# Performance work log

Measured on AMD Instinct MI355X. Metric: run time of the kernel, lower is better.

## Reference

```python
import jax, jax.numpy as jnp
import numpy as np

B, D, H, W, C = 2, 8, 56, 56, 384
NH = 12
HD = C // NH
WIN = (2, 7, 7)
SHIFT = (1, 3, 3)
TDIM = 384
RANK = C // 8
HID = 4 * C
N = WIN[0] * WIN[1] * WIN[2]  # 98 tokens per window
NW = (D // WIN[0]) * (H // WIN[1]) * (W // WIN[2])  # windows per batch element


def _rel_index():
    wd, wh, ww = WIN
    coords = np.stack(np.meshgrid(np.arange(wd), np.arange(wh), np.arange(ww), indexing='ij'))
    coords = coords.reshape(3, -1)  # (3, N)
    rel = (coords[:, :, None] - coords[:, None, :]).transpose(1, 2, 0)  # (N, N, 3)
    rel[..., 0] += wd - 1; rel[..., 1] += wh - 1; rel[..., 2] += ww - 1
    rel[..., 0] *= (2 * wh - 1) * (2 * ww - 1)
    rel[..., 1] *= (2 * ww - 1)
    return rel.sum(-1)  # (N, N) int

REL_IDX = _rel_index()


def _wpart_np(x):
    b, d, h, w, c = x.shape
    x = x.reshape(b, d // WIN[0], WIN[0], h // WIN[1], WIN[1], w // WIN[2], WIN[2], c)
    return x.transpose(0, 1, 3, 5, 2, 4, 6, 7).reshape(-1, N, c)


def _attn_mask():
    # faithful port of compute_mask (note: only 2 slices along W, as in source)
    wd, wh, ww = WIN
    sd, sh, sw = SHIFT
    img = np.zeros((1, D, H, W, 1), np.float32)
    cnt = 0
    for ds in (slice(-wd), slice(-wd, -sd), slice(-sd, None)):
        for hs in (slice(-wh), slice(-wh, -sh), slice(-sh, None)):
            for ws in (slice(-ww), slice(-ww, None)):
                img[:, ds, hs, ws, :] = cnt
                cnt += 1
    mw = _wpart_np(img).squeeze(-1)  # (nW, N)
    am = mw[:, None, :] - mw[:, :, None]  # (nW, N, N)
    return np.where(am != 0, np.float32(-100.0), np.float32(0.0))

ATTN_MASK = _attn_mask()


def wpart(x):
    b, c = x.shape[0], x.shape[-1]
    x = x.reshape(b, D // WIN[0], WIN[0], H // WIN[1], WIN[1], W // WIN[2], WIN[2], c)
    return x.transpose(0, 1, 3, 5, 2, 4, 6, 7).reshape(-1, N, c)


def wrev(win):
    c = win.shape[-1]
    x = win.reshape(B, D // WIN[0], H // WIN[1], W // WIN[2], WIN[0], WIN[1], WIN[2], c)
    return x.transpose(0, 1, 4, 2, 5, 3, 6, 7).reshape(B, D, H, W, c)


def ln(x):
    m = x.mean(-1, keepdims=True)
    v = ((x - m) ** 2).mean(-1, keepdims=True)
    return (x - m) / jnp.sqrt(v + 1e-6)


def window_attn(xw, qkv_w, qkv_b, proj_w, proj_b, rel_bias, mask):
    Bw = xw.shape[0]
    qkv = (xw @ qkv_w + qkv_b).reshape(Bw, N, 3, NH, HD).transpose(2, 0, 3, 1, 4)
    q, k, v = qkv[0] * (HD ** -0.5), qkv[1], qkv[2]
    a = jnp.einsum('bhnd,bhmd->bhnm', q, k)  # (Bw, NH, N, N)
    bias = rel_bias[REL_IDX.reshape(-1)].reshape(N, N, NH).transpose(2, 0, 1)
    a = a + bias[None]
    a = a.reshape(Bw // NW, NW, NH, N, N) + mask[None, :, None]
    a = jax.nn.softmax(a.reshape(Bw, NH, N, N), axis=-1)
    out = jnp.einsum('bhnm,bhmd->bhnd', a, v).transpose(0, 2, 1, 3).reshape(Bw, N, C)
    return out @ proj_w + proj_b


def setup_inputs() -> dict:
    key = jax.random.key(0)
    ks = jax.random.split(key, 16)
    s = 0.02
    return {
        'x': jax.random.normal(ks[0], (B, D, H, W, C), jnp.float32),
        't': jax.random.normal(ks[1], (B, TDIM), jnp.float32),
        'qkv_w': jax.random.normal(ks[2], (C, 3 * C), jnp.float32) * s,
        'qkv_b': jax.random.normal(ks[3], (3 * C,), jnp.float32) * s,
        'proj_w': jax.random.normal(ks[4], (C, C), jnp.float32) * s,
        'proj_b': jax.random.normal(ks[5], (C,), jnp.float32) * s,
        'rel_bias': jax.random.normal(ks[6], ((2 * WIN[0] - 1) * (2 * WIN[1] - 1) * (2 * WIN[2] - 1), NH), jnp.float32) * s,
        'fc1_w': jax.random.normal(ks[7], (C, HID), jnp.float32) * s,
        'fc1_b': jax.random.normal(ks[8], (HID,), jnp.float32) * s,
        'fc2_w': jax.random.normal(ks[9], (HID, C), jnp.float32) * s,
        'fc2_b': jax.random.normal(ks[10], (C,), jnp.float32) * s,
        'ada_w1': jax.random.normal(ks[11], (TDIM, RANK), jnp.float32) * s,
        'ada_w2': jax.random.normal(ks[12], (RANK, 6 * C), jnp.float32) * s,
        'ada_b2': jax.random.normal(ks[13], (6 * C,), jnp.float32) * s,
    }


def reference(x, t, qkv_w, qkv_b, proj_w, proj_b, rel_bias, fc1_w, fc1_b, fc2_w, fc2_b, ada_w1, ada_w2, ada_b2):
    mask = jnp.asarray(ATTN_MASK)
    mod = jax.nn.silu(t) @ ada_w1 @ ada_w2 + ada_b2  # (B, 6C)
    s_msa, sc_msa, g_msa, s_mlp, sc_mlp, g_mlp = jnp.split(mod, 6, axis=1)

    def mod5(h, sh, sc):
        return h * (1 + sc[:, None, None, None, :]) + sh[:, None, None, None, :]

    # attention branch (shifted-window MSA)
    h = mod5(ln(x), s_msa, sc_msa)
    hs = jnp.roll(h, shift=(-SHIFT[0], -SHIFT[1], -SHIFT[2]), axis=(1, 2, 3))
    aw = window_attn(wpart(hs), qkv_w, qkv_b, proj_w, proj_b, rel_bias, mask)
    hs = wrev(aw)
    h = jnp.roll(hs, shift=SHIFT, axis=(1, 2, 3))
    x = x + g_msa[:, None, None, None, :] * h

    # MLP branch
    h2 = mod5(ln(x), s_mlp, sc_mlp)
    m = jax.nn.gelu(h2 @ fc1_w + fc1_b, approximate=False) @ fc2_w + fc2_b
    return x + g_mlp[:, None, None, None, :] * m
```

## Files before the change

### kernel.cpp

```cpp
#include <hip/hip_runtime.h>
#include <hip/hip_bf16.h>
#include <math.h>

using bf16 = __hip_bfloat16;
typedef __bf16 bf16x8 __attribute__((ext_vector_type(8)));
typedef float f32x4 __attribute__((ext_vector_type(4)));
typedef unsigned int u32;


__device__ __forceinline__ void async_cp16(const void* g, void* l) {
  __builtin_amdgcn_global_load_lds(
      (const __attribute__((address_space(1))) u32*)g,
      (__attribute__((address_space(3))) u32*)l, 16, 0, 0);
}

__device__ __forceinline__ int row_to_gidx(int row) {
  int win = row / 98, tok = row - win * 98;
  int b = win >> 8, wd = (win >> 6) & 3, wh = (win >> 3) & 7, ww = win & 7;
  int td = tok / 49, rem = tok - td * 49;
  int th = rem / 7, tw = rem - th * 7;
  int od = (wd * 2 + td + 1) & 7;
  int oh = wh * 7 + th + 3; if (oh >= 56) oh -= 56;
  int ow = ww * 7 + tw + 3; if (ow >= 56) ow -= 56;
  return ((b * 8 + od) * 56 + oh) * 56 + ow;
}

__global__ __launch_bounds__(256) void mod_kernel(
    const float* __restrict__ t, const float* __restrict__ w1,
    const float* __restrict__ w2, const float* __restrict__ b2,
    float* __restrict__ modout)
{
  __shared__ float u[2 * 48];
  int tid = threadIdx.x;
  if (tid < 96) {
    int b = tid / 48, r = tid - (tid / 48) * 48;
    float acc = 0.f;
    for (int k = 0; k < 384; ++k) {
      float x = t[b * 384 + k];
      float s = x / (1.f + __expf(-x));
      acc += s * w1[k * 48 + r];
    }
    u[b * 48 + r] = acc;
  }
  __syncthreads();
  for (int idx = tid; idx < 2 * 2304; idx += 256) {
    int b = idx / 2304, c = idx - b * 2304;
    float acc = b2[c];
    #pragma unroll
    for (int k = 0; k < 48; ++k) acc += u[b * 48 + k] * w2[k * 2304 + c];
    modout[idx] = acc;
  }
}

__global__ __launch_bounds__(256) void wconv_kernel(
    const float* __restrict__ W, bf16* __restrict__ Wt, int K, int N)
{
  int idx = blockIdx.x * 256 + threadIdx.x;
  if (idx < K * N) {
    int k = idx / N, n = idx - k * N;
    Wt[(size_t)n * K + k] = __float2bfloat16(W[idx]);
  }
}

__global__ __launch_bounds__(256) void bm_kernel(
    const float* __restrict__ relb, bf16* __restrict__ bm)
{
  int idx = blockIdx.x * 256 + threadIdx.x;
  if (idx >= 4 * 12 * 112 * 112) return;
  int j = idx % 112, tmp = idx / 112;
  int i = tmp % 112; tmp /= 112;
  int h = tmp % 12, p = tmp / 12;
  float v;
  if (i < 98 && j < 98) {
    int tdi = i / 49, ri = i % 49, thi = ri / 7, twi = ri % 7;
    int tdj = j / 49, rj = j % 49, thj = rj / 7, twj = rj % 7;
    int ridx = (tdi - tdj + 1) * 169 + (thi - thj + 6) * 13 + (twi - twj + 6);
    bool msk = ((p & 2) && (tdi != tdj)) || ((p & 1) && ((thi < 4) != (thj < 4)));
    v = relb[ridx * 12 + h] + (msk ? -100.f : 0.f);
  } else {
    v = -1e38f;
  }
  bm[idx] = __float2bfloat16(v);
}

template <int PHASE>
__global__ __launch_bounds__(256) void ln_mod_kernel(
    const float* __restrict__ src, const float* __restrict__ modv,
    bf16* __restrict__ dst)
{
  int wid = threadIdx.x >> 6, lane = threadIdx.x & 63;
  int row = blockIdx.x * 4 + wid;
  int gtok;
  if (PHASE == 0) gtok = row_to_gidx(row); else gtok = row;
  int b = row / 25088;
  const float* s = src + (size_t)gtok * 384;
  float vals[6], sum = 0.f, sq = 0.f;
  #pragma unroll
  for (int i = 0; i < 6; ++i) {
    float v = s[lane + i * 64];
    vals[i] = v; sum += v; sq += v * v;
  }
  #pragma unroll
  for (int o = 32; o; o >>= 1) { sum += __shfl_xor(sum, o, 64); sq += __shfl_xor(sq, o, 64); }
  float mean = sum * (1.f / 384.f);
  float var = sq * (1.f / 384.f) - mean * mean;
  float rstd = rsqrtf(var + 1e-6f);
  int mb = b * 2304 + (PHASE == 0 ? 0 : 1152);
  #pragma unroll
  for (int i = 0; i < 6; ++i) {
    int c = lane + i * 64;
    float scv = modv[mb + 384 + c], shv = modv[mb + c];
    dst[(size_t)row * 384 + c] = __float2bfloat16((vals[i] - mean) * rstd * (1.f + scv) + shv);
  }
}

template <int EPI>
__global__ __launch_bounds__(256) void gemm128_kernel(
    const bf16* __restrict__ A, const bf16* __restrict__ Bt,
    const float* __restrict__ bias, const int N, const int K,
    bf16* __restrict__ outB, float* __restrict__ outF,
    const float* __restrict__ resid, const float* __restrict__ modv)
{
  __shared__ bf16 sA[2][128 * 32];
  __shared__ bf16 sB[2][128 * 32];
  const int tid = threadIdx.x;
  const int lane = tid & 63, wid = tid >> 6;
  const int wm = wid >> 1, wn = wid & 1;

  const int gx = gridDim.x;
  const int nwg = gx * (int)gridDim.y;
  const int orig = (int)blockIdx.y * gx + (int)blockIdx.x;
  const int q = nwg >> 3;
  const int wg = (orig & 7) * q + (orig >> 3);
  const int bx = wg % gx, by = wg / gx;
  const int row0 = by * 128, col0 = bx * 128;

  const int lrow = lane & 15;
  const int sl8 = (((lane >> 4) ^ ((lane >> 1) & 3)) << 3);
  const int r0 = tid >> 2;
  const int c0 = (((tid & 3) ^ ((tid >> 3) & 3)) << 3);

  const f32x4 vzero = {0.f, 0.f, 0.f, 0.f};
  f32x4 acc[4][4];
  #pragma unroll
  for (int m = 0; m < 4; ++m)
    #pragma unroll
    for (int n = 0; n < 4; ++n) acc[m][n] = vzero;

  const bf16* Arow0 = A + (size_t)(row0 + r0) * K + c0;
  const bf16* Arow1 = A + (size_t)(row0 + r0 + 64) * K + c0;
  const bf16* Brow0 = Bt + (size_t)(col0 + r0) * K + c0;
  const bf16* Brow1 = Bt + (size_t)(col0 + r0 + 64) * K + c0;

  auto stage = [&](int b, int kt) {
    async_cp16(Arow0 + kt, &sA[b][(size_t)tid * 8]);
    async_cp16(Arow1 + kt, &sA[b][(size_t)(tid + 256) * 8]);
    async_cp16(Brow0 + kt, &sB[b][(size_t)tid * 8]);
    async_cp16(Brow1 + kt, &sB[b][(size_t)(tid + 256) * 8]);
  };
  auto compute = [&](int cb) {
    bf16x8 af[4], bfv[4];
    #pragma unroll
    for (int m = 0; m < 4; ++m)
      af[m] = *(const bf16x8*)(&sA[cb][(wm * 64 + m * 16 + lrow) * 32 + sl8]);
    #pragma unroll
    for (int n = 0; n < 4; ++n)
      bfv[n] = *(const bf16x8*)(&sB[cb][(wn * 64 + n * 16 + lrow) * 32 + sl8]);
    #pragma unroll
    for (int m = 0; m < 4; ++m)
      #pragma unroll
      for (int n = 0; n < 4; ++n)
        acc[m][n] = __builtin_amdgcn_mfma_f32_16x16x32_bf16(af[m], bfv[n], acc[m][n], 0, 0, 0);
  };

  stage(0, 0);
  asm volatile("s_waitcnt vmcnt(0)" ::: "memory");
  __syncthreads();
  int cur = 0;
  for (int kt = 32; kt < K; kt += 32) {
    stage(cur ^ 1, kt);
    compute(cur);
    asm volatile("s_waitcnt vmcnt(0)" ::: "memory");
    __syncthreads();
    cur ^= 1;
  }
  compute(cur);

  #pragma unroll
  for (int m = 0; m < 4; ++m) {
    #pragma unroll
    for (int r = 0; r < 4; ++r) {
      const int row = row0 + wm * 64 + m * 16 + (lane >> 4) * 4 + r;
      int gofs = 0, b = 0;
      if (EPI == 1) { gofs = row_to_gidx(row) * 384; b = row / 25088; }
      if (EPI == 3) { gofs = row * 384; b = row / 25088; }
      #pragma unroll
      for (int n = 0; n < 4; ++n) {
        const int col = col0 + wn * 64 + n * 16 + (lane & 15);
        float v = acc[m][n][r] + bias[col];
        if (EPI == 0) {
          outB[(size_t)row * N + col] = __float2bfloat16(v);
        } else if (EPI == 2) {
          float g = 0.5f * v * (1.f + erff(v * 0.70710678118654752f));
          outB[(size_t)row * N + col] = __float2bfloat16(g);
        } else if (EPI == 1) {
          outF[gofs + col] = resid[gofs + col] + modv[b * 2304 + 768 + col] * v;
        } else {
          outF[gofs + col] = resid[gofs + col] + modv[b * 2304 + 1920 + col] * v;
        }
      }
    }
  }
}

__global__ __launch_bounds__(256) void attn_kernel(
    const bf16* __restrict__ qkv, const bf16* __restrict__ bm,
    bf16* __restrict__ outp)
{
  __shared__ bf16 k_s[112][40];
  __shared__ bf16 v_t[32][136];
  __shared__ bf16 p_s[4][16][136];

  const int head = blockIdx.x;
  const int win = blockIdx.y;
  const int tid = threadIdx.x;
  const int lane = tid & 63, wid = tid >> 6;
  const int g = lane >> 4, c16 = lane & 15;
  const size_t rowbase = (size_t)win * 98;
  const bf16 zero = __float2bfloat16(0.f);

  for (int lin = tid; lin < 448; lin += 256) {
    int row = lin >> 2, ch = (lin & 3) << 3;
    uint4 val = make_uint4(0, 0, 0, 0);
    if (row < 98)
      val = *(const uint4*)(qkv + (rowbase + row) * 1152 + 384 + head * 32 + ch);
    *(uint4*)&k_s[row][ch] = val;
  }
  for (int lin = tid; lin < 4096; lin += 256) {
    int d = lin & 31, tok = lin >> 5;
    bf16 val = zero;
    if (tok < 98) val = qkv[(rowbase + tok) * 1152 + 768 + head * 32 + d];
    v_t[d][tok] = val;
  }
  for (int lin = tid; lin < 1536; lin += 256) {
    int w = lin / 384, rem = lin - w * 384;
    p_s[w][rem / 24][112 + rem % 24] = zero;
  }
  __syncthreads();

  const int p = ((((win >> 6) & 3) == 3) ? 2 : 0) | ((((win >> 3) & 7) == 7) ? 1 : 0);
  const bf16* bmrow = bm + (size_t)(p * 12 + head) * 12544;
  const float scale = 0.17677669529663687f;
  const f32x4 vzero = {0.f, 0.f, 0.f, 0.f};

  for (int s = wid; s < 7; s += 4) {
    const int q0 = s * 16;
    int qrow = q0 + c16; if (qrow > 97) qrow = 97;
    bf16x8 qf = *(const bf16x8*)(qkv + (rowbase + qrow) * 1152 + head * 32 + g * 8);

    f32x4 sa[7];
    #pragma unroll
    for (int ct = 0; ct < 7; ++ct) {
      bf16x8 kf = *(const bf16x8*)&k_s[ct * 16 + c16][g * 8];
      sa[ct] = __builtin_amdgcn_mfma_f32_16x16x32_bf16(qf, kf, vzero, 0, 0, 0);
    }

    float sv[7][4];
    float mrow[4] = {-1e30f, -1e30f, -1e30f, -1e30f};
    #pragma unroll
    for (int ct = 0; ct < 7; ++ct) {
      #pragma unroll
      for (int r = 0; r < 4; ++r) {
        int i = q0 + g * 4 + r, j = ct * 16 + c16;
        float val = sa[ct][r] * scale + __bfloat162float(bmrow[i * 112 + j]);
        sv[ct][r] = val;
        mrow[r] = fmaxf(mrow[r], val);
      }
    }
    #pragma unroll
    for (int r = 0; r < 4; ++r) {
      #pragma unroll
      for (int off = 1; off < 16; off <<= 1)
        mrow[r] = fmaxf(mrow[r], __shfl_xor(mrow[r], off, 64));
    }
    float rsum[4] = {0.f, 0.f, 0.f, 0.f};
    #pragma unroll
    for (int ct = 0; ct < 7; ++ct) {
      #pragma unroll
      for (int r = 0; r < 4; ++r) {
        float e = __expf(sv[ct][r] - mrow[r]);
        sv[ct][r] = e;
        rsum[r] += e;
      }
    }
    #pragma unroll
    for (int r = 0; r < 4; ++r) {
      #pragma unroll
      for (int off = 1; off < 16; off <<= 1)
        rsum[r] += __shfl_xor(rsum[r], off, 64);
      rsum[r] = 1.f / rsum[r];
    }
    #pragma unroll
    for (int ct = 0; ct < 7; ++ct)
      #pragma unroll
      for (int r = 0; r < 4; ++r)
        p_s[wid][g * 4 + r][ct * 16 + c16] = __float2bfloat16(sv[ct][r] * rsum[r]);

    asm volatile("s_waitcnt lgkmcnt(0)" ::: "memory");

    f32x4 o0 = vzero, o1 = vzero;
    #pragma unroll
    for (int kk = 0; kk < 4; ++kk) {
      bf16x8 pa = *(const bf16x8*)&p_s[wid][c16][kk * 32 + g * 8];
      bf16x8 v0 = *(const bf16x8*)&v_t[c16][kk * 32 + g * 8];
      bf16x8 v1 = *(const bf16x8*)&v_t[16 + c16][kk * 32 + g * 8];
      o0 = __builtin_amdgcn_mfma_f32_16x16x32_bf16(pa, v0, o0, 0, 0, 0);
      o1 = __builtin_amdgcn_mfma_f32_16x16x32_bf16(pa, v1, o1, 0, 0, 0);
    }
    #pragma unroll
    for (int r = 0; r < 4; ++r) {
      int qi = q0 + g * 4 + r;
      if (qi < 98) {
        size_t ob = (rowbase + qi) * 384 + head * 32;
        outp[ob + c16] = __float2bfloat16(o0[r]);
        outp[ob + 16 + c16] = __float2bfloat16(o1[r]);
      }
    }
  }
}

extern "C" void kernel_launch(void* const* d_in, const int* in_sizes, int n_in,
                              void* d_out, int out_size, void* d_ws, size_t ws_size,
                              hipStream_t stream)
{
  (void)in_sizes; (void)n_in; (void)out_size; (void)ws_size;
  const float* x      = (const float*)d_in[0];
  const float* t      = (const float*)d_in[1];
  const float* qkv_w  = (const float*)d_in[2];
  const float* qkv_b  = (const float*)d_in[3];
  const float* proj_w = (const float*)d_in[4];
  const float* proj_b = (const float*)d_in[5];
  const float* relb   = (const float*)d_in[6];
  const float* fc1_w  = (const float*)d_in[7];
  const float* fc1_b  = (const float*)d_in[8];
  const float* fc2_w  = (const float*)d_in[9];
  const float* fc2_b  = (const float*)d_in[10];
  const float* ada_w1 = (const float*)d_in[11];
  const float* ada_w2 = (const float*)d_in[12];
  const float* ada_b2 = (const float*)d_in[13];
  float* out = (float*)d_out;
  char* ws = (char*)d_ws;

  float* modbuf = (float*)(ws + 0);
  bf16* wqkv_t  = (bf16*)(ws + 18432);
  bf16* wproj_t = (bf16*)(ws + 903168);
  bf16* wfc1_t  = (bf16*)(ws + 1198080);
  bf16* wfc2_t  = (bf16*)(ws + 2377728);
  bf16* bufA    = (bf16*)(ws + 3557376);
  bf16* qkvbuf  = (bf16*)(ws + 42092544);
  bf16* bufB    = (bf16*)(ws + 42092544 + 115605504);
  bf16* midbuf  = (bf16*)(ws + 42092544);
  bf16* bmbuf   = bufA;

  wconv_kernel<<<(384 * 1152 + 255) / 256, 256, 0, stream>>>(qkv_w, wqkv_t, 384, 1152);
  wconv_kernel<<<(384 * 384 + 255) / 256, 256, 0, stream>>>(proj_w, wproj_t, 384, 384);
  wconv_kernel<<<(384 * 1536 + 255) / 256, 256, 0, stream>>>(fc1_w, wfc1_t, 384, 1536);
  wconv_kernel<<<(1536 * 384 + 255) / 256, 256, 0, stream>>>(fc2_w, wfc2_t, 1536, 384);

  mod_kernel<<<1, 256, 0, stream>>>(t, ada_w1, ada_w2, ada_b2, modbuf);

  ln_mod_kernel<0><<<12544, 256, 0, stream>>>(x, modbuf, bufA);

  gemm128_kernel<0><<<dim3(9, 392), 256, 0, stream>>>(bufA, wqkv_t, qkv_b, 1152, 384,
                                                      qkvbuf, nullptr, nullptr, nullptr);

  bm_kernel<<<2352, 256, 0, stream>>>(relb, bmbuf);

  attn_kernel<<<dim3(12, 512), 256, 0, stream>>>(qkvbuf, bmbuf, bufB);

  gemm128_kernel<1><<<dim3(3, 392), 256, 0, stream>>>(bufB, wproj_t, proj_b, 384, 384,
                                                      nullptr, out, x, modbuf);

  ln_mod_kernel<1><<<12544, 256, 0, stream>>>(out, modbuf, bufA);

  gemm128_kernel<2><<<dim3(12, 392), 256, 0, stream>>>(bufA, wfc1_t, fc1_b, 1536, 384,
                                                       midbuf, nullptr, nullptr, nullptr);

  gemm128_kernel<3><<<dim3(3, 392), 256, 0, stream>>>(midbuf, wfc2_t, fc2_b, 384, 1536,
                                                      nullptr, out, out, modbuf);
}
```

Before: 566.2 us.

## Triple-buffer GEMM K-loop, transpose MFMA operands for vectorized epilogue stores

```diff
diff --git a/kernel.cpp b/kernel.cpp
--- a/kernel.cpp
+++ b/kernel.cpp
@@ -4,6 +4,7 @@
 
 using bf16 = __hip_bfloat16;
 typedef __bf16 bf16x8 __attribute__((ext_vector_type(8)));
+typedef __bf16 bf16x4 __attribute__((ext_vector_type(4)));
 typedef float f32x4 __attribute__((ext_vector_type(4)));
 typedef unsigned int u32;
 
@@ -115,14 +116,14 @@
 }
 
 template <int EPI>
-__global__ __launch_bounds__(256) void gemm128_kernel(
+__global__ __launch_bounds__(256, 3) void gemm128_kernel(
     const bf16* __restrict__ A, const bf16* __restrict__ Bt,
     const float* __restrict__ bias, const int N, const int K,
     bf16* __restrict__ outB, float* __restrict__ outF,
     const float* __restrict__ resid, const float* __restrict__ modv)
 {
-  __shared__ bf16 sA[2][128 * 32];
-  __shared__ bf16 sB[2][128 * 32];
+  __shared__ bf16 sA[3][128 * 32];
+  __shared__ bf16 sB[3][128 * 32];
   const int tid = threadIdx.x;
   const int lane = tid & 63, wid = tid >> 6;
   const int wm = wid >> 1, wn = wid & 1;
@@ -130,8 +131,9 @@
   const int gx = gridDim.x;
   const int nwg = gx * (int)gridDim.y;
   const int orig = (int)blockIdx.y * gx + (int)blockIdx.x;
-  const int q = nwg >> 3;
-  const int wg = (orig & 7) * q + (orig >> 3);
+  const int q = nwg >> 3, rr = nwg & 7;
+  const int xcd = orig & 7, idx = orig >> 3;
+  const int wg = (xcd < rr ? xcd * (q + 1) : rr * (q + 1) + (xcd - rr) * q) + idx;
   const int bx = wg % gx, by = wg / gx;
   const int row0 = by * 128, col0 = bx * 128;
 
@@ -170,44 +172,61 @@
     for (int m = 0; m < 4; ++m)
       #pragma unroll
       for (int n = 0; n < 4; ++n)
-        acc[m][n] = __builtin_amdgcn_mfma_f32_16x16x32_bf16(af[m], bfv[n], acc[m][n], 0, 0, 0);
+        acc[m][n] = __builtin_amdgcn_mfma_f32_16x16x32_bf16(bfv[n], af[m], acc[m][n], 0, 0, 0);
   };
 
+  const int nk = K >> 5;
   stage(0, 0);
-  asm volatile("s_waitcnt vmcnt(0)" ::: "memory");
-  __syncthreads();
-  int cur = 0;
-  for (int kt = 32; kt < K; kt += 32) {
-    stage(cur ^ 1, kt);
-    compute(cur);
-    asm volatile("s_waitcnt vmcnt(0)" ::: "memory");
-    __syncthreads();
-    cur ^= 1;
-  }
-  compute(cur);
-
+  stage(1, 32);
+  int cb = 0, st = 2;
+  for (int t = 0; t < nk; ++t) {
+    if (t + 1 < nk) asm volatile("s_waitcnt vmcnt(4)" ::: "memory");
+    else            asm volatile("s_waitcnt vmcnt(0)" ::: "memory");
+    __builtin_amdgcn_s_barrier();
+    __builtin_amdgcn_sched_barrier(0);
+    if (t + 2 < nk) {
+      stage(st, (t + 2) * 32);
+      st = (st == 2) ? 0 : st + 1;
+    }
+    compute(cb);
+    cb = (cb == 2) ? 0 : cb + 1;
+  }
+
+  const int cg = (lane >> 4) << 2;
   #pragma unroll
   for (int m = 0; m < 4; ++m) {
-    #pragma unroll
-    for (int r = 0; r < 4; ++r) {
-      const int row = row0 + wm * 64 + m * 16 + (lane >> 4) * 4 + r;
-      int gofs = 0, b = 0;
-      if (EPI == 1) { gofs = row_to_gidx(row) * 384; b = row / 25088; }
-      if (EPI == 3) { gofs = row * 384; b = row / 25088; }
-      #pragma unroll
-      for (int n = 0; n < 4; ++n) {
-        const int col = col0 + wn * 64 + n * 16 + (lane & 15);
-        float v = acc[m][n][r] + bias[col];
-        if (EPI == 0) {
-          outB[(size_t)row * N + col] = __float2bfloat16(v);
-        } else if (EPI == 2) {
-          float g = 0.5f * v * (1.f + erff(v * 0.70710678118654752f));
-          outB[(size_t)row * N + col] = __float2bfloat16(g);
-        } else if (EPI == 1) {
-          outF[gofs + col] = resid[gofs + col] + modv[b * 2304 + 768 + col] * v;
-        } else {
-          outF[gofs + col] = resid[gofs + col] + modv[b * 2304 + 1920 + col] * v;
+    const int row = row0 + wm * 64 + m * 16 + lrow;
+    int gofs = 0, b = 0;
+    if (EPI == 1) { gofs = row_to_gidx(row) * 384; b = row / 25088; }
+    if (EPI == 3) { gofs = row * 384; b = row / 25088; }
+    #pragma unroll
+    for (int n = 0; n < 4; ++n) {
+      const int colb = col0 + wn * 64 + n * 16 + cg;
+      const f32x4 bi = *(const f32x4*)(bias + colb);
+      f32x4 v;
+      #pragma unroll
+      for (int r = 0; r < 4; ++r) v[r] = acc[m][n][r] + bi[r];
+      if (EPI == 0) {
+        bf16x4 pk;
+        #pragma unroll
+        for (int r = 0; r < 4; ++r) pk[r] = (__bf16)v[r];
+        *(bf16x4*)(outB + (size_t)row * N + colb) = pk;
+      } else if (EPI == 2) {
+        bf16x4 pk;
+        #pragma unroll
+        for (int r = 0; r < 4; ++r) {
+          float g = 0.5f * v[r] * (1.f + erff(v[r] * 0.70710678118654752f));
+          pk[r] = (__bf16)g;
         }
+        *(bf16x4*)(outB + (size_t)row * N + colb) = pk;
+      } else {
+        const int mo = b * 2304 + (EPI == 1 ? 768 : 1920);
+        const f32x4 res = *(const f32x4*)(resid + gofs + colb);
+        const f32x4 gm = *(const f32x4*)(modv + mo + colb);
+        f32x4 o;
+        #pragma unroll
+        for (int r = 0; r < 4; ++r) o[r] = res[r] + gm[r] * v[r];
+        *(f32x4*)(outF + gofs + colb) = o;
       }
     }
   }
```

Result: slower. 585.7 us (+3.4%).

## Fuse QKV projection GEMM into windowed attention kernel per window

Applied to the files above, without the earlier changes.

```diff
diff --git a/kernel.cpp b/kernel.cpp
--- a/kernel.cpp
+++ b/kernel.cpp
@@ -213,119 +213,180 @@
   }
 }
 
-__global__ __launch_bounds__(256) void attn_kernel(
-    const bf16* __restrict__ qkv, const bf16* __restrict__ bm,
+__global__ __launch_bounds__(256) void qkv_attn_kernel(
+    const bf16* __restrict__ A, const bf16* __restrict__ Wqkv,
+    const float* __restrict__ qkv_b, const bf16* __restrict__ bm,
     bf16* __restrict__ outp)
 {
+  __shared__ bf16 q_s[112][40];
   __shared__ bf16 k_s[112][40];
   __shared__ bf16 v_t[32][136];
   __shared__ bf16 p_s[4][16][136];
 
-  const int head = blockIdx.x;
-  const int win = blockIdx.y;
+  const int win = blockIdx.x;
   const int tid = threadIdx.x;
   const int lane = tid & 63, wid = tid >> 6;
   const int g = lane >> 4, c16 = lane & 15;
   const size_t rowbase = (size_t)win * 98;
   const bf16 zero = __float2bfloat16(0.f);
-
-  for (int lin = tid; lin < 448; lin += 256) {
-    int row = lin >> 2, ch = (lin & 3) << 3;
-    uint4 val = make_uint4(0, 0, 0, 0);
-    if (row < 98)
-      val = *(const uint4*)(qkv + (rowbase + row) * 1152 + 384 + head * 32 + ch);
-    *(uint4*)&k_s[row][ch] = val;
-  }
-  for (int lin = tid; lin < 4096; lin += 256) {
-    int d = lin & 31, tok = lin >> 5;
-    bf16 val = zero;
-    if (tok < 98) val = qkv[(rowbase + tok) * 1152 + 768 + head * 32 + d];
-    v_t[d][tok] = val;
-  }
+  const f32x4 vzero = {0.f, 0.f, 0.f, 0.f};
+
+  for (int lin = tid; lin < 768; lin += 256)
+    v_t[lin / 24][112 + lin % 24] = zero;
   for (int lin = tid; lin < 1536; lin += 256) {
     int w = lin / 384, rem = lin - w * 384;
     p_s[w][rem / 24][112 + rem % 24] = zero;
   }
+
+  bf16x8 af[2][12];
+  #pragma unroll
+  for (int si = 0; si < 2; ++si) {
+    const int s = wid + si * 4;
+    int srow = s * 16 + c16; if (srow > 97) srow = 97;
+    const bf16* ap = A + (rowbase + srow) * 384 + g * 8;
+    #pragma unroll
+    for (int ks = 0; ks < 12; ++ks)
+      af[si][ks] = *(const bf16x8*)(ap + ks * 32);
+  }
+
+  const int p = ((((win >> 6) & 3) == 3) ? 2 : 0) | ((((win >> 3) & 7) == 7) ? 1 : 0);
+  const float scale = 0.17677669529663687f;
+
   __syncthreads();
 
-  const int p = ((((win >> 6) & 3) == 3) ? 2 : 0) | ((((win >> 3) & 7) == 7) ? 1 : 0);
-  const bf16* bmrow = bm + (size_t)(p * 12 + head) * 12544;
-  const float scale = 0.17677669529663687f;
-  const f32x4 vzero = {0.f, 0.f, 0.f, 0.f};
-
-  for (int s = wid; s < 7; s += 4) {
-    const int q0 = s * 16;
-    int qrow = q0 + c16; if (qrow > 97) qrow = 97;
-    bf16x8 qf = *(const bf16x8*)(qkv + (rowbase + qrow) * 1152 + head * 32 + g * 8);
-
-    f32x4 sa[7];
-    #pragma unroll
-    for (int ct = 0; ct < 7; ++ct) {
-      bf16x8 kf = *(const bf16x8*)&k_s[ct * 16 + c16][g * 8];
-      sa[ct] = __builtin_amdgcn_mfma_f32_16x16x32_bf16(qf, kf, vzero, 0, 0, 0);
+  for (int h = 0; h < 12; ++h) {
+    f32x4 acc[2][3][2];
+    #pragma unroll
+    for (int si = 0; si < 2; ++si)
+      #pragma unroll
+      for (int mat = 0; mat < 3; ++mat)
+        #pragma unroll
+        for (int nt = 0; nt < 2; ++nt) acc[si][mat][nt] = vzero;
+
+    const bf16* wp = Wqkv + ((size_t)(h * 32 + c16)) * 384 + g * 8;
+    #pragma unroll
+    for (int ks = 0; ks < 12; ++ks) {
+      bf16x8 bfr[3][2];
+      #pragma unroll
+      for (int mat = 0; mat < 3; ++mat)
+        #pragma unroll
+        for (int nt = 0; nt < 2; ++nt)
+          bfr[mat][nt] = *(const bf16x8*)(wp + (size_t)(mat * 384 + nt * 16) * 384 + ks * 32);
+      #pragma unroll
+      for (int si = 0; si < 2; ++si)
+        #pragma unroll
+        for (int mat = 0; mat < 3; ++mat)
+          #pragma unroll
+          for (int nt = 0; nt < 2; ++nt)
+            acc[si][mat][nt] = __builtin_amdgcn_mfma_f32_16x16x32_bf16(
+                af[si][ks], bfr[mat][nt], acc[si][mat][nt], 0, 0, 0);
     }
 
-    float sv[7][4];
-    float mrow[4] = {-1e30f, -1e30f, -1e30f, -1e30f};
-    #pragma unroll
-    for (int ct = 0; ct < 7; ++ct) {
+    #pragma unroll
+    for (int si = 0; si < 2; ++si) {
+      const int s = wid + si * 4;
+      if (s < 7) {
+        #pragma unroll
+        for (int mat = 0; mat < 3; ++mat) {
+          const float b0 = qkv_b[mat * 384 + h * 32 + c16];
+          const float b1 = qkv_b[mat * 384 + h * 32 + 16 + c16];
+          #pragma unroll
+          for (int r = 0; r < 4; ++r) {
+            const int tok = s * 16 + g * 4 + r;
+            const float v0 = acc[si][mat][0][r] + b0;
+            const float v1 = acc[si][mat][1][r] + b1;
+            if (mat == 0) {
+              q_s[tok][c16] = __float2bfloat16(v0);
+              q_s[tok][16 + c16] = __float2bfloat16(v1);
+            } else if (mat == 1) {
+              k_s[tok][c16] = __float2bfloat16(v0);
+              k_s[tok][16 + c16] = __float2bfloat16(v1);
+            } else {
+              const bool ok = tok < 98;
+              v_t[c16][tok] = ok ? __float2bfloat16(v0) : zero;
+              v_t[16 + c16][tok] = ok ? __float2bfloat16(v1) : zero;
+            }
+          }
+        }
+      }
+    }
+    __syncthreads();
+
+    const bf16* bmrow = bm + (size_t)(p * 12 + h) * 12544;
+    for (int s = wid; s < 7; s += 4) {
+      const int q0 = s * 16;
+      bf16x8 qf = *(const bf16x8*)&q_s[q0 + c16][g * 8];
+
+      f32x4 sa[7];
+      #pragma unroll
+      for (int ct = 0; ct < 7; ++ct) {
+        bf16x8 kf = *(const bf16x8*)&k_s[ct * 16 + c16][g * 8];
+        sa[ct] = __builtin_amdgcn_mfma_f32_16x16x32_bf16(qf, kf, vzero, 0, 0, 0);
+      }
+
+      float sv[7][4];
+      float mrow[4] = {-1e30f, -1e30f, -1e30f, -1e30f};
+      #pragma unroll
+      for (int ct = 0; ct < 7; ++ct) {
+        #pragma unroll
+        for (int r = 0; r < 4; ++r) {
+          int i = q0 + g * 4 + r, j = ct * 16 + c16;
+          float val = sa[ct][r] * scale + __bfloat162float(bmrow[i * 112 + j]);
+          sv[ct][r] = val;
+          mrow[r] = fmaxf(mrow[r], val);
+        }
+      }
       #pragma unroll
       for (int r = 0; r < 4; ++r) {
-        int i = q0 + g * 4 + r, j = ct * 16 + c16;
-        float val = sa[ct][r] * scale + __bfloat162float(bmrow[i * 112 + j]);
-        sv[ct][r] = val;
-        mrow[r] = fmaxf(mrow[r], val);
+        #pragma unroll
+        for (int off = 1; off < 16; off <<= 1)
+          mrow[r] = fmaxf(mrow[r], __shfl_xor(mrow[r], off, 64));
+      }
+      float rsum[4] = {0.f, 0.f, 0.f, 0.f};
+      #pragma unroll
+      for (int ct = 0; ct < 7; ++ct) {
+        #pragma unroll
+        for (int r = 0; r < 4; ++r) {
+          float e = __expf(sv[ct][r] - mrow[r]);
+          sv[ct][r] = e;
+          rsum[r] += e;
+        }
+      }
+      #pragma unroll
+      for (int r = 0; r < 4; ++r) {
+        #pragma unroll
+        for (int off = 1; off < 16; off <<= 1)
+          rsum[r] += __shfl_xor(rsum[r], off, 64);
+        rsum[r] = 1.f / rsum[r];
+      }
+      #pragma unroll
+      for (int ct = 0; ct < 7; ++ct)
+        #pragma unroll
+        for (int r = 0; r < 4; ++r)
+          p_s[wid][g * 4 + r][ct * 16 + c16] = __float2bfloat16(sv[ct][r] * rsum[r]);
+
+      asm volatile("s_waitcnt lgkmcnt(0)" ::: "memory");
+
+      f32x4 o0 = vzero, o1 = vzero;
+      #pragma unroll
+      for (int kk = 0; kk < 4; ++kk) {
+        bf16x8 pa = *(const bf16x8*)&p_s[wid][c16][kk * 32 + g * 8];
+        bf16x8 v0 = *(const bf16x8*)&v_t[c16][kk * 32 + g * 8];
+        bf16x8 v1 = *(const bf16x8*)&v_t[16 + c16][kk * 32 + g * 8];
+        o0 = __builtin_amdgcn_mfma_f32_16x16x32_bf16(pa, v0, o0, 0, 0, 0);
+        o1 = __builtin_amdgcn_mfma_f32_16x16x32_bf16(pa, v1, o1, 0, 0, 0);
+      }
+      #pragma unroll
+      for (int r = 0; r < 4; ++r) {
+        int qi = q0 + g * 4 + r;
+        if (qi < 98) {
+          size_t ob = (rowbase + qi) * 384 + h * 32;
+          outp[ob + c16] = __float2bfloat16(o0[r]);
+          outp[ob + 16 + c16] = __float2bfloat16(o1[r]);
+        }
       }
     }
-    #pragma unroll
-    for (int r = 0; r < 4; ++r) {
-      #pragma unroll
-      for (int off = 1; off < 16; off <<= 1)
-        mrow[r] = fmaxf(mrow[r], __shfl_xor(mrow[r], off, 64));
-    }
-    float rsum[4] = {0.f, 0.f, 0.f, 0.f};
-    #pragma unroll
-    for (int ct = 0; ct < 7; ++ct) {
-      #pragma unroll
-      for (int r = 0; r < 4; ++r) {
-        float e = __expf(sv[ct][r] - mrow[r]);
-        sv[ct][r] = e;
-        rsum[r] += e;
-      }
-    }
-    #pragma unroll
-    for (int r = 0; r < 4; ++r) {
-      #pragma unroll
-      for (int off = 1; off < 16; off <<= 1)
-        rsum[r] += __shfl_xor(rsum[r], off, 64);
-      rsum[r] = 1.f / rsum[r];
-    }
-    #pragma unroll
-    for (int ct = 0; ct < 7; ++ct)
-      #pragma unroll
-      for (int r = 0; r < 4; ++r)
-        p_s[wid][g * 4 + r][ct * 16 + c16] = __float2bfloat16(sv[ct][r] * rsum[r]);
-
-    asm volatile("s_waitcnt lgkmcnt(0)" ::: "memory");
-
-    f32x4 o0 = vzero, o1 = vzero;
-    #pragma unroll
-    for (int kk = 0; kk < 4; ++kk) {
-      bf16x8 pa = *(const bf16x8*)&p_s[wid][c16][kk * 32 + g * 8];
-      bf16x8 v0 = *(const bf16x8*)&v_t[c16][kk * 32 + g * 8];
-      bf16x8 v1 = *(const bf16x8*)&v_t[16 + c16][kk * 32 + g * 8];
-      o0 = __builtin_amdgcn_mfma_f32_16x16x32_bf16(pa, v0, o0, 0, 0, 0);
-      o1 = __builtin_amdgcn_mfma_f32_16x16x32_bf16(pa, v1, o1, 0, 0, 0);
-    }
-    #pragma unroll
-    for (int r = 0; r < 4; ++r) {
-      int qi = q0 + g * 4 + r;
-      if (qi < 98) {
-        size_t ob = (rowbase + qi) * 384 + head * 32;
-        outp[ob + c16] = __float2bfloat16(o0[r]);
-        outp[ob + 16 + c16] = __float2bfloat16(o1[r]);
-      }
-    }
+    __syncthreads();
   }
 }
 
@@ -357,10 +418,9 @@
   bf16* wfc1_t  = (bf16*)(ws + 1198080);
   bf16* wfc2_t  = (bf16*)(ws + 2377728);
   bf16* bufA    = (bf16*)(ws + 3557376);
-  bf16* qkvbuf  = (bf16*)(ws + 42092544);
-  bf16* bufB    = (bf16*)(ws + 42092544 + 115605504);
+  bf16* bufB    = (bf16*)(ws + 42092544);
   bf16* midbuf  = (bf16*)(ws + 42092544);
-  bf16* bmbuf   = bufA;
+  bf16* bmbuf   = (bf16*)(ws + 195028992);
 
   wconv_kernel<<<(384 * 1152 + 255) / 256, 256, 0, stream>>>(qkv_w, wqkv_t, 384, 1152);
   wconv_kernel<<<(384 * 384 + 255) / 256, 256, 0, stream>>>(proj_w, wproj_t, 384, 384);
@@ -368,15 +428,11 @@
   wconv_kernel<<<(1536 * 384 + 255) / 256, 256, 0, stream>>>(fc2_w, wfc2_t, 1536, 384);
 
   mod_kernel<<<1, 256, 0, stream>>>(t, ada_w1, ada_w2, ada_b2, modbuf);
+  bm_kernel<<<2352, 256, 0, stream>>>(relb, bmbuf);
 
   ln_mod_kernel<0><<<12544, 256, 0, stream>>>(x, modbuf, bufA);
 
-  gemm128_kernel<0><<<dim3(9, 392), 256, 0, stream>>>(bufA, wqkv_t, qkv_b, 1152, 384,
-                                                      qkvbuf, nullptr, nullptr, nullptr);
-
-  bm_kernel<<<2352, 256, 0, stream>>>(relb, bmbuf);
-
-  attn_kernel<<<dim3(12, 512), 256, 0, stream>>>(qkvbuf, bmbuf, bufB);
+  qkv_attn_kernel<<<512, 256, 0, stream>>>(bufA, wqkv_t, qkv_b, bmbuf, bufB);
 
   gemm128_kernel<1><<<dim3(3, 392), 256, 0, stream>>>(bufB, wproj_t, proj_b, 384, 384,
                                                       nullptr, out, x, modbuf);
```

Result: slower. 735.7 us (+29.9%).

## Pre-pack weights into MFMA fragment layout and load B directly from global

Applied to the files above, without the earlier changes.

```diff
diff --git a/kernel.cpp b/kernel.cpp
--- a/kernel.cpp
+++ b/kernel.cpp
@@ -52,14 +52,16 @@
   }
 }
 
-__global__ __launch_bounds__(256) void wconv_kernel(
-    const float* __restrict__ W, bf16* __restrict__ Wt, int K, int N)
+__global__ __launch_bounds__(256) void wconv_frag_kernel(
+    const float* __restrict__ W, bf16* __restrict__ Wf, int K, int N)
 {
   int idx = blockIdx.x * 256 + threadIdx.x;
-  if (idx < K * N) {
-    int k = idx / N, n = idx - k * N;
-    Wt[(size_t)n * K + k] = __float2bfloat16(W[idx]);
-  }
+  if (idx >= K * N) return;
+  int k = idx / N, n = idx - (idx / N) * N;
+  int ntile = n >> 4, kstep = k >> 5;
+  int l = (n & 15) + (((k >> 3) & 3) << 4);
+  size_t dst = (((size_t)(ntile * (K >> 5) + kstep)) << 9) + (l << 3) + (k & 7);
+  Wf[dst] = __float2bfloat16(W[idx]);
 }
 
 __global__ __launch_bounds__(256) void bm_kernel(
@@ -116,13 +118,12 @@
 
 template <int EPI>
 __global__ __launch_bounds__(256) void gemm128_kernel(
-    const bf16* __restrict__ A, const bf16* __restrict__ Bt,
+    const bf16* __restrict__ A, const bf16* __restrict__ Bf,
     const float* __restrict__ bias, const int N, const int K,
     bf16* __restrict__ outB, float* __restrict__ outF,
     const float* __restrict__ resid, const float* __restrict__ modv)
 {
   __shared__ bf16 sA[2][128 * 32];
-  __shared__ bf16 sB[2][128 * 32];
   const int tid = threadIdx.x;
   const int lane = tid & 63, wid = tid >> 6;
   const int wm = wid >> 1, wn = wid & 1;
@@ -140,6 +141,14 @@
   const int r0 = tid >> 2;
   const int c0 = (((tid & 3) ^ ((tid >> 3) & 3)) << 3);
 
+  const int nK32 = K >> 5;
+  const bf16* Bfb[4];
+  #pragma unroll
+  for (int n = 0; n < 4; ++n) {
+    const int ntile = (col0 >> 4) + wn * 4 + n;
+    Bfb[n] = Bf + (((size_t)(ntile * nK32)) << 9) + (lane << 3);
+  }
+
   const f32x4 vzero = {0.f, 0.f, 0.f, 0.f};
   f32x4 acc[4][4];
   #pragma unroll
@@ -149,42 +158,36 @@
 
   const bf16* Arow0 = A + (size_t)(row0 + r0) * K + c0;
   const bf16* Arow1 = A + (size_t)(row0 + r0 + 64) * K + c0;
-  const bf16* Brow0 = Bt + (size_t)(col0 + r0) * K + c0;
-  const bf16* Brow1 = Bt + (size_t)(col0 + r0 + 64) * K + c0;
 
   auto stage = [&](int b, int kt) {
     async_cp16(Arow0 + kt, &sA[b][(size_t)tid * 8]);
     async_cp16(Arow1 + kt, &sA[b][(size_t)(tid + 256) * 8]);
-    async_cp16(Brow0 + kt, &sB[b][(size_t)tid * 8]);
-    async_cp16(Brow1 + kt, &sB[b][(size_t)(tid + 256) * 8]);
-  };
-  auto compute = [&](int cb) {
-    bf16x8 af[4], bfv[4];
-    #pragma unroll
-    for (int m = 0; m < 4; ++m)
-      af[m] = *(const bf16x8*)(&sA[cb][(wm * 64 + m * 16 + lrow) * 32 + sl8]);
-    #pragma unroll
-    for (int n = 0; n < 4; ++n)
-      bfv[n] = *(const bf16x8*)(&sB[cb][(wn * 64 + n * 16 + lrow) * 32 + sl8]);
-    #pragma unroll
-    for (int m = 0; m < 4; ++m)
-      #pragma unroll
-      for (int n = 0; n < 4; ++n)
-        acc[m][n] = __builtin_amdgcn_mfma_f32_16x16x32_bf16(af[m], bfv[n], acc[m][n], 0, 0, 0);
   };
 
   stage(0, 0);
   asm volatile("s_waitcnt vmcnt(0)" ::: "memory");
   __syncthreads();
   int cur = 0;
-  for (int kt = 32; kt < K; kt += 32) {
-    stage(cur ^ 1, kt);
-    compute(cur);
-    asm volatile("s_waitcnt vmcnt(0)" ::: "memory");
-    __syncthreads();
-    cur ^= 1;
-  }
-  compute(cur);
+  for (int t = 0; t < nK32; ++t) {
+    bf16x8 bfv[4], af[4];
+    #pragma unroll
+    for (int n = 0; n < 4; ++n)
+      bfv[n] = *(const bf16x8*)(Bfb[n] + ((size_t)t << 9));
+    if (t + 1 < nK32) stage(cur ^ 1, (t + 1) * 32);
+    #pragma unroll
+    for (int m = 0; m < 4; ++m)
+      af[m] = *(const bf16x8*)(&sA[cur][(wm * 64 + m * 16 + lrow) * 32 + sl8]);
+    #pragma unroll
+    for (int m = 0; m < 4; ++m)
+      #pragma unroll
+      for (int n = 0; n < 4; ++n)
+        acc[m][n] = __builtin_amdgcn_mfma_f32_16x16x32_bf16(af[m], bfv[n], acc[m][n], 0, 0, 0);
+    if (t + 1 < nK32) {
+      asm volatile("s_waitcnt vmcnt(0)" ::: "memory");
+      __syncthreads();
+      cur ^= 1;
+    }
+  }
 
   #pragma unroll
   for (int m = 0; m < 4; ++m) {
@@ -362,10 +365,10 @@
   bf16* midbuf  = (bf16*)(ws + 42092544);
   bf16* bmbuf   = bufA;
 
-  wconv_kernel<<<(384 * 1152 + 255) / 256, 256, 0, stream>>>(qkv_w, wqkv_t, 384, 1152);
-  wconv_kernel<<<(384 * 384 + 255) / 256, 256, 0, stream>>>(proj_w, wproj_t, 384, 384);
-  wconv_kernel<<<(384 * 1536 + 255) / 256, 256, 0, stream>>>(fc1_w, wfc1_t, 384, 1536);
-  wconv_kernel<<<(1536 * 384 + 255) / 256, 256, 0, stream>>>(fc2_w, wfc2_t, 1536, 384);
+  wconv_frag_kernel<<<(384 * 1152 + 255) / 256, 256, 0, stream>>>(qkv_w, wqkv_t, 384, 1152);
+  wconv_frag_kernel<<<(384 * 384 + 255) / 256, 256, 0, stream>>>(proj_w, wproj_t, 384, 384);
+  wconv_frag_kernel<<<(384 * 1536 + 255) / 256, 256, 0, stream>>>(fc1_w, wfc1_t, 384, 1536);
+  wconv_frag_kernel<<<(1536 * 384 + 255) / 256, 256, 0, stream>>>(fc2_w, wfc2_t, 1536, 384);
 
   mod_kernel<<<1, 256, 0, stream>>>(t, ada_w1, ada_w2, ada_b2, modbuf);
 
```

Result: no change. 574.5 us (+1.5%).
